# Performance work log

Measured on AMD Instinct MI355X. Metric: run time of the kernel, lower is better.

The kernel has to match this reference:

```python
import jax, jax.numpy as jnp
import numpy as np

# Static problem sizes (equal-sized graphs; unbatch+pad of edge_RWSE then reduces to a reshape,
# which is exactly what reshape_flattened_adj computes in that case).
_B, _N, _K, _EMB_HALF, _NUM_TYPES, _E = 8, 512, 16, 32, 5, 32768


def setup_inputs() -> dict:
    key = jax.random.key(0)
    k1, k2, k3, k4, k5, k6, k7 = jax.random.split(key, 7)
    # node -> graph assignment (ordered), B graphs of N nodes each
    node_batch = jnp.repeat(jnp.arange(_B, dtype=jnp.int64), _N)
    # edges: both endpoints inside the same graph, no self loops (module adds its own)
    g = jax.random.randint(k1, (_E,), 0, _B)
    src_l = jax.random.randint(k2, (_E,), 0, _N)
    dst_l = (src_l + jax.random.randint(k3, (_E,), 1, _N)) % _N
    edge_index = jnp.stack([g * _N + src_l, g * _N + dst_l]).astype(jnp.int64)
    # edge types in [0, num_types-2] so edge_attr+1 (and self-loop value 1) index the table
    edge_attr = jax.random.randint(k4, (_E,), 0, _NUM_TYPES - 1).astype(jnp.int64)
    # flattened dense RWSE edge features: [sum(N_i^2), K]
    edge_RWSE = jax.random.normal(k5, (_B * _N * _N, _K), dtype=jnp.float32)
    # learned params: Embedding(num_types, emb_dim//2) and Linear(K, emb_dim//2)
    emb_table = 0.02 * jax.random.normal(k6, (_NUM_TYPES, _EMB_HALF), dtype=jnp.float32)
    W = jax.random.normal(k7, (_K, _EMB_HALF), dtype=jnp.float32) / np.sqrt(_K)
    b = jnp.zeros((_EMB_HALF,), dtype=jnp.float32)
    return {"edge_RWSE": edge_RWSE, "emb_table": emb_table, "W": W, "b": b,
            "edge_index": edge_index, "edge_attr": edge_attr, "node_batch": node_batch,
            "B": _B, "N_max": _N}


def reference(edge_RWSE, emb_table, W, b, edge_index, edge_attr, node_batch, B, N_max):
    n_total = node_batch.shape[0]
    # per-graph local node indices (node_batch is ordered, as PyG requires)
    counts = jax.ops.segment_sum(jnp.ones((n_total,), jnp.int32), node_batch, num_segments=B)
    starts = jnp.concatenate([jnp.zeros((1,), jnp.int32), jnp.cumsum(counts)[:-1]])
    local = jnp.arange(n_total, dtype=jnp.int32) - starts[node_batch]

    # --- TypeDictEdgeEncoder: to_dense_adj(add_self_loops(edge_attr+1, fill=1)) then embed ---
    src, dst = edge_index[0], edge_index[1]
    g = node_batch[src]
    A = jnp.zeros((B, N_max, N_max), jnp.int32)
    A = A.at[g, local[src], local[dst]].add(edge_attr.astype(jnp.int32) + 1)
    A = A.at[node_batch, local, local].add(1)  # self-loop type = fill_diagonal = 1
    type_dense = emb_table[A]                      # [B, Nm, Nm, emb//2]
    edge_attr_emb = emb_table[edge_attr]           # [E, emb//2]

    # --- RWSEEdgeEncoder: ragged->padded dense (equal sizes => reshape) + Linear ---
    pe_dense = edge_RWSE.reshape(B, N_max, N_max, -1) @ W + b  # [B, Nm, Nm, emb//2]

    edge_dense = jnp.concatenate([type_dense, pe_dense], axis=-1)  # [B, Nm, Nm, emb]
    return edge_dense, edge_attr_emb
```

## Files before the change

kernel.cpp:

```cpp
#include <hip/hip_runtime.h>
#include <hip/hip_bf16.h>

#define B_   8
#define N_   512
#define K_   16
#define EH_  32
#define NT_  5
#define E_   32768
#define P_   (B_ * N_ * N_)

__global__ __launch_bounds__(256) void scatter_k(const int* __restrict__ ei,
                                                 const int* __restrict__ ea,
                                                 int* __restrict__ A) {
    int t = blockIdx.x * 256 + threadIdx.x;
    if (t < E_) {
        int s = ei[t];
        int d = ei[E_ + t];
        int g  = s >> 9;
        int ls = s & (N_ - 1);
        int ld = d & (N_ - 1);
        atomicAdd(&A[(g * N_ + ls) * N_ + ld], ea[t] + 1);
    } else {
        int n = t - E_;
        if (n < B_ * N_) {
            int g = n >> 9;
            int l = n & (N_ - 1);
            atomicAdd(&A[(g * N_ + l) * N_ + l], 1);
        }
    }
}

#define PPB 256
__global__ __launch_bounds__(256) void fuse_k(const float* __restrict__ rwse,
                                              const float* __restrict__ emb,
                                              const float* __restrict__ W,
                                              const float* __restrict__ bias,
                                              const int* __restrict__ A,
                                              float* __restrict__ out) {
    __shared__ float semb[NT_][EH_];
    __shared__ float sW[K_][EH_];
    __shared__ float sb[EH_];

    const int tid = threadIdx.x;
    for (int i = tid; i < K_ * EH_; i += 256) sW[i >> 5][i & 31] = W[i];
    if (tid < NT_ * EH_) semb[tid >> 5][tid & 31] = emb[tid];
    if (tid < EH_) sb[tid] = bias[tid];
    __syncthreads();

    const int j = tid & 15;
    const int c = (j - 8) * 4;

    float4 wc[K_];
    float4 bv = {0.f, 0.f, 0.f, 0.f};
    if (j >= 8) {
        #pragma unroll
        for (int k = 0; k < K_; ++k)
            wc[k] = *(const float4*)&sW[k][c];
        bv = *(const float4*)&sb[c];
    }

    const long base = (long)blockIdx.x * PPB;
    #pragma unroll 1
    for (int it = 0; it < PPB / 16; ++it) {
        const long pair = base + it * 16 + (tid >> 4);
        int a = A[pair];
        a = (a < NT_) ? a : (NT_ - 1);
        float4 o;
        if (j < 8) {
            o = *(const float4*)&semb[a][j * 4];
        } else {
            const float4* rw = (const float4*)(rwse + pair * K_);
            float r[K_];
            *(float4*)&r[0]  = rw[0];
            *(float4*)&r[4]  = rw[1];
            *(float4*)&r[8]  = rw[2];
            *(float4*)&r[12] = rw[3];
            float4 acc = bv;
            #pragma unroll
            for (int k = 0; k < K_; ++k) {
                acc.x = fmaf(r[k], wc[k].x, acc.x);
                acc.y = fmaf(r[k], wc[k].y, acc.y);
                acc.z = fmaf(r[k], wc[k].z, acc.z);
                acc.w = fmaf(r[k], wc[k].w, acc.w);
            }
            o = acc;
        }
        ((float4*)out)[pair * 16 + j] = o;
    }
}

__global__ __launch_bounds__(256) void attr_k(const float* __restrict__ emb,
                                              const int* __restrict__ ea,
                                              float* __restrict__ out2) {
    int t = blockIdx.x * 256 + threadIdx.x;
    int e = t >> 5, cc = t & 31;
    out2[t] = emb[ea[e] * EH_ + cc];
}

extern "C" void kernel_launch(void* const* d_in, const int* in_sizes, int n_in,
                              void* d_out, int out_size, void* d_ws, size_t ws_size,
                              hipStream_t stream) {
    const float* rwse = (const float*)d_in[0];
    const float* emb  = (const float*)d_in[1];
    const float* W    = (const float*)d_in[2];
    const float* bias = (const float*)d_in[3];
    const int*   ei   = (const int*)d_in[4];
    const int*   ea   = (const int*)d_in[5];

    int*   A    = (int*)d_ws;
    float* out  = (float*)d_out;
    float* out2 = out + (long)P_ * 64;

    hipMemsetAsync(A, 0, (size_t)P_ * sizeof(int), stream);
    scatter_k<<<(E_ + B_ * N_ + 255) / 256, 256, 0, stream>>>(ei, ea, A);
    fuse_k<<<P_ / PPB, 256, 0, stream>>>(rwse, emb, W, bias, A, out);
    attr_k<<<(E_ * EH_) / 256, 256, 0, stream>>>(emb, ea, out2);
}
```

Measured before the change: 822.8 us.

## Fuse attr gather into scatter, stage A in LDS, use nontemporal loads/stores

```diff
diff --git a/kernel.cpp b/kernel.cpp
--- a/kernel.cpp
+++ b/kernel.cpp
@@ -9,10 +9,18 @@
 #define E_   32768
 #define P_   (B_ * N_ * N_)
 
-__global__ __launch_bounds__(256) void scatter_k(const int* __restrict__ ei,
-                                                 const int* __restrict__ ea,
-                                                 int* __restrict__ A) {
+typedef __attribute__((ext_vector_type(4))) float f32x4;
+
+__global__ __launch_bounds__(256) void prep_k(const int* __restrict__ ei,
+                                              const int* __restrict__ ea,
+                                              const float* __restrict__ emb,
+                                              int* __restrict__ A,
+                                              f32x4* __restrict__ out2) {
     int t = blockIdx.x * 256 + threadIdx.x;
+    if (t < E_ * (EH_ / 4)) {
+        int e = t >> 3, c4 = t & 7;
+        out2[e * 8 + c4] = ((const f32x4*)emb)[ea[e] * 8 + c4];
+    }
     if (t < E_) {
         int s = ei[t];
         int d = ei[E_ + t];
@@ -20,13 +28,9 @@
         int ls = s & (N_ - 1);
         int ld = d & (N_ - 1);
         atomicAdd(&A[(g * N_ + ls) * N_ + ld], ea[t] + 1);
-    } else {
+    } else if (t - E_ < B_ * N_) {
         int n = t - E_;
-        if (n < B_ * N_) {
-            int g = n >> 9;
-            int l = n & (N_ - 1);
-            atomicAdd(&A[(g * N_ + l) * N_ + l], 1);
-        }
+        atomicAdd(&A[n * N_ + (n & (N_ - 1))], 1);
     }
 }
 
@@ -40,61 +44,68 @@
     __shared__ float semb[NT_][EH_];
     __shared__ float sW[K_][EH_];
     __shared__ float sb[EH_];
+    __shared__ int   sA[PPB];
 
     const int tid = threadIdx.x;
+    const long base = (long)blockIdx.x * PPB;
+
     for (int i = tid; i < K_ * EH_; i += 256) sW[i >> 5][i & 31] = W[i];
     if (tid < NT_ * EH_) semb[tid >> 5][tid & 31] = emb[tid];
     if (tid < EH_) sb[tid] = bias[tid];
+    {
+        int a = A[base + tid];
+        sA[tid] = (a < NT_) ? a : (NT_ - 1);
+    }
     __syncthreads();
 
     const int j = tid & 15;
     const int c = (j - 8) * 4;
 
-    float4 wc[K_];
-    float4 bv = {0.f, 0.f, 0.f, 0.f};
+    f32x4 wc[K_];
+    f32x4 bv = {0.f, 0.f, 0.f, 0.f};
     if (j >= 8) {
         #pragma unroll
         for (int k = 0; k < K_; ++k)
-            wc[k] = *(const float4*)&sW[k][c];
-        bv = *(const float4*)&sb[c];
+            wc[k] = *(const f32x4*)&sW[k][c];
+        bv = *(const f32x4*)&sb[c];
     }
 
-    const long base = (long)blockIdx.x * PPB;
-    #pragma unroll 1
+    f32x4* __restrict__ outv = (f32x4*)out;
+    #pragma unroll 2
     for (int it = 0; it < PPB / 16; ++it) {
-        const long pair = base + it * 16 + (tid >> 4);
-        int a = A[pair];
-        a = (a < NT_) ? a : (NT_ - 1);
-        float4 o;
+        const int  lp   = it * 16 + (tid >> 4);
+        const long pair = base + lp;
+        f32x4 o;
         if (j < 8) {
-            o = *(const float4*)&semb[a][j * 4];
+            int a = sA[lp];
+            o = *(const f32x4*)&semb[a][j * 4];
         } else {
-            const float4* rw = (const float4*)(rwse + pair * K_);
-            float r[K_];
-            *(float4*)&r[0]  = rw[0];
-            *(float4*)&r[4]  = rw[1];
-            *(float4*)&r[8]  = rw[2];
-            *(float4*)&r[12] = rw[3];
-            float4 acc = bv;
+            const f32x4* rw = (const f32x4*)(rwse + pair * K_);
+            f32x4 acc = bv;
             #pragma unroll
-            for (int k = 0; k < K_; ++k) {
-                acc.x = fmaf(r[k], wc[k].x, acc.x);
-                acc.y = fmaf(r[k], wc[k].y, acc.y);
-                acc.z = fmaf(r[k], wc[k].z, acc.z);
-                acc.w = fmaf(r[k], wc[k].w, acc.w);
+            for (int kk = 0; kk < 4; ++kk) {
+                f32x4 rv = __builtin_nontemporal_load(&rw[kk]);
+                acc.x = fmaf(rv.x, wc[4*kk+0].x, acc.x);
+                acc.y = fmaf(rv.x, wc[4*kk+0].y, acc.y);
+                acc.z = fmaf(rv.x, wc[4*kk+0].z, acc.z);
+                acc.w = fmaf(rv.x, wc[4*kk+0].w, acc.w);
+                acc.x = fmaf(rv.y, wc[4*kk+1].x, acc.x);
+                acc.y = fmaf(rv.y, wc[4*kk+1].y, acc.y);
+                acc.z = fmaf(rv.y, wc[4*kk+1].z, acc.z);
+                acc.w = fmaf(rv.y, wc[4*kk+1].w, acc.w);
+                acc.x = fmaf(rv.z, wc[4*kk+2].x, acc.x);
+                acc.y = fmaf(rv.z, wc[4*kk+2].y, acc.y);
+                acc.z = fmaf(rv.z, wc[4*kk+2].z, acc.z);
+                acc.w = fmaf(rv.z, wc[4*kk+2].w, acc.w);
+                acc.x = fmaf(rv.w, wc[4*kk+3].x, acc.x);
+                acc.y = fmaf(rv.w, wc[4*kk+3].y, acc.y);
+                acc.z = fmaf(rv.w, wc[4*kk+3].z, acc.z);
+                acc.w = fmaf(rv.w, wc[4*kk+3].w, acc.w);
             }
             o = acc;
         }
-        ((float4*)out)[pair * 16 + j] = o;
+        __builtin_nontemporal_store(o, &outv[pair * 16 + j]);
     }
-}
-
-__global__ __launch_bounds__(256) void attr_k(const float* __restrict__ emb,
-                                              const int* __restrict__ ea,
-                                              float* __restrict__ out2) {
-    int t = blockIdx.x * 256 + threadIdx.x;
-    int e = t >> 5, cc = t & 31;
-    out2[t] = emb[ea[e] * EH_ + cc];
 }
 
 extern "C" void kernel_launch(void* const* d_in, const int* in_sizes, int n_in,
@@ -109,10 +120,10 @@
 
     int*   A    = (int*)d_ws;
     float* out  = (float*)d_out;
-    float* out2 = out + (long)P_ * 64;
+    f32x4* out2 = (f32x4*)(out + (long)P_ * 64);
 
     hipMemsetAsync(A, 0, (size_t)P_ * sizeof(int), stream);
-    scatter_k<<<(E_ + B_ * N_ + 255) / 256, 256, 0, stream>>>(ei, ea, A);
+    int prep_threads = E_ * (EH_ / 4);
+    prep_k<<<(prep_threads + 255) / 256, 256, 0, stream>>>(ei, ea, emb, A, out2);
     fuse_k<<<P_ / PPB, 256, 0, stream>>>(rwse, emb, W, bias, A, out);
-    attr_k<<<(E_ * EH_) / 256, 256, 0, stream>>>(emb, ea, out2);
 }
```

Result: faster. 721.6 us (-12.3%).
